# Kernel optimization log

Hardware: AMD Instinct MI355X
Metric: run time of the kernel (lower is better)

Reference implementation:

```python
import jax, jax.numpy as jnp
import numpy as np

E = 1024; H = 16; D = E // H; L = 16
B = 4; TB = 1024; TW = 512
SCALE = D ** -0.5


def _rel_matrix(S):
    r = jnp.arange(S)
    return jnp.clip(r[None, :] - r[:, None], -L, L) + L  # [S,S] ints in [0, 2L]


def _heads(x):
    # [T, b, E] -> [b*H, T, D]
    T, b, _ = x.shape
    return x.reshape(T, b * H, D).transpose(1, 0, 2)


def _rel_logits(q, table, S):
    # Shaw-style relative-key logits without materializing [S,S,D] embeddings:
    # q: [n, S, D], table: [2L+1, D] -> [n, S, S]
    mat = _rel_matrix(S)                          # [S, S]
    all_r = jnp.einsum('ntd,rd->ntr', q, table)   # [n, S, 2L+1]
    return jnp.take_along_axis(all_r, mat[None, :, :], axis=2)


def setup_inputs() -> dict:
    key = jax.random.key(0)
    ks = jax.random.split(key, 10)
    s = 0.02
    w = lambda k, shape: jax.random.normal(k, shape, jnp.float32) * s
    return {
        'query_bpe': jax.random.normal(ks[0], (TB, B, E), jnp.float32),
        'query_word': jax.random.normal(ks[1], (TW, B, E), jnp.float32),
        'mapping': jax.random.uniform(ks[2], (B, TB, TW), jnp.float32),
        'Wq_bpe': w(ks[3], (E, E)), 'bq_bpe': jnp.zeros((E,), jnp.float32),
        'Wk_bpe': w(ks[4], (E, E)), 'bk_bpe': jnp.zeros((E,), jnp.float32),
        'Wq_word': w(ks[5], (E, E)), 'bq_word': jnp.zeros((E,), jnp.float32),
        'Wk_word': w(ks[6], (E, E)), 'bk_word': jnp.zeros((E,), jnp.float32),
        'Wv': w(ks[7], (E, E)), 'bv': jnp.zeros((E,), jnp.float32),
        'Wo': w(ks[8], (E, E)), 'bo': jnp.zeros((E,), jnp.float32),
        'rel_keys_bpe': w(ks[9], (2 * L + 1, D)),
    }


def reference(query_bpe, query_word, mapping, Wq_bpe, bq_bpe, Wk_bpe, bk_bpe,
              Wq_word, bq_word, Wk_word, bk_word, Wv, bv, Wo, bo, rel_keys_bpe):
    b = query_bpe.shape[1]
    q_bpe = _heads((query_bpe @ Wq_bpe.T + bq_bpe) * SCALE)    # [bH, TB, D]
    k_bpe = _heads(query_bpe @ Wk_bpe.T + bk_bpe)
    q_word = _heads((query_word @ Wq_word.T + bq_word) * SCALE)  # [bH, TW, D]
    k_word = _heads(query_word @ Wk_word.T + bk_word)
    v = _heads(query_bpe @ Wv.T + bv)
    # content + relative-position logits for both streams
    # (k_only path in source looks up relative_position_keys_bpe for BOTH streams)
    attn_bpe = q_bpe @ k_bpe.transpose(0, 2, 1) + _rel_logits(q_bpe, rel_keys_bpe, TB)
    attn_word = q_word @ k_word.transpose(0, 2, 1) + _rel_logits(q_word, rel_keys_bpe, TW)
    aw = attn_word.reshape(b, H, TW, TW)
    # fuse word-level scores into BPE positions via alignment mapping: M A M^T
    fused = jnp.einsum('bqw,bhws->bhqs', mapping, aw)
    fused = jnp.einsum('bhqs,bks->bhqk', fused, mapping)
    attn = attn_bpe.reshape(b, H, TB, TB) + fused
    probs = jax.nn.softmax(attn, axis=-1)
    out = jnp.einsum('bhqk,bhkd->bhqd', probs, v.reshape(b, H, TB, D))
    out = out.transpose(2, 0, 1, 3).reshape(TB, b, E)  # back to [T, B, E]
    return out @ Wo.T + bo
```

## Files before the change

kernel.cpp:

```cpp
#include <hip/hip_runtime.h>


#define DEV __device__ __forceinline__
#define GAS(x) ((const __attribute__((address_space(1))) unsigned*)(x))
#define LAS(x) ((__attribute__((address_space(3))) unsigned*)(x))

typedef unsigned short u16;
typedef __attribute__((ext_vector_type(8))) short short8;
typedef __attribute__((ext_vector_type(8))) _Float16 half8;
typedef __attribute__((ext_vector_type(4))) float floatx4;

DEV float bf2f(u16 u) { union { unsigned u; float f; } v; v.u = ((unsigned)u) << 16; return v.f; }
DEV u16 f2bf(float f) {
  union { float f; unsigned u; } v; v.f = f;
  unsigned r = v.u + 0x7FFFu + ((v.u >> 16) & 1u);
  return (u16)(r >> 16);
}
DEV u16 f2h_bits(float f) { union { _Float16 h; u16 u; } v; v.h = (_Float16)f; return v.u; }

template <int N> DEV void vmwait() {
  asm volatile("s_waitcnt vmcnt(%0)" ::"n"(N) : "memory");
  __builtin_amdgcn_sched_barrier(0);
}
DEV void barrier_raw() {
  asm volatile("" ::: "memory");
  __builtin_amdgcn_s_barrier();
  asm volatile("" ::: "memory");
}

DEV void stage_u16(const u16* g, int ld, u16* lds, int tid) {
#pragma unroll
  for (int p = 0; p < 2; ++p) {
    int o = (p * 256 + tid) * 16;
    int r = o >> 6, c = (o >> 4) & 3, sc = c ^ ((r >> 1) & 3);
    __builtin_amdgcn_global_load_lds(GAS(g + (size_t)r * ld + sc * 8),
                                     LAS((char*)lds + o), 16, 0, 0);
  }
}

DEV void stage_u16_half(const u16* g, int ld, u16* lds, int tid, int p) {
  int o = (p * 256 + tid) * 16;
  int r = o >> 6, c = (o >> 4) & 3, sc = c ^ ((r >> 1) & 3);
  __builtin_amdgcn_global_load_lds(GAS(g + (size_t)(r - p * 64) * ld + sc * 8),
                                   LAS((char*)lds + o), 16, 0, 0);
}

DEV void stage_f32_bf(const float* g, int ld, u16* lds, int tid) {
#pragma unroll
  for (int p = 0; p < 2; ++p) {
    int o = (p * 256 + tid) * 16;
    int r = o >> 6, c = (o >> 4) & 3, sc = c ^ ((r >> 1) & 3);
    const float* src = g + (size_t)r * ld + sc * 8;
    union { short8 s; u16 u[8]; } oh;
#pragma unroll
    for (int j = 0; j < 8; ++j) oh.u[j] = f2bf(src[j]);
    *(short8*)((char*)lds + o) = oh.s;
  }
}

DEV void stage_f32_split(const float* g, int ld, u16* ldsh, u16* ldsl, int tid) {
#pragma unroll
  for (int p = 0; p < 2; ++p) {
    int o = (p * 256 + tid) * 16;
    int r = o >> 6, c = (o >> 4) & 3, sc = c ^ ((r >> 1) & 3);
    const float* src = g + (size_t)r * ld + sc * 8;
    union { short8 s; u16 u[8]; } oh, ol;
#pragma unroll
    for (int j = 0; j < 8; ++j) {
      float f = src[j];
      u16 h = f2bf(f);
      oh.u[j] = h;
      ol.u[j] = f2bf(f - bf2f(h));
    }
    *(short8*)((char*)ldsh + o) = oh.s;
    *(short8*)((char*)ldsl + o) = ol.s;
  }
}

DEV short8 frag_ld(const u16* lds, int row, int quad) {
  int c = quad ^ ((row >> 1) & 3);
  return *(const short8*)(lds + row * 32 + c * 8);
}

DEV void mma_bf16(const u16* As, const u16* Bs, int wr, int wc, int m, int quad, floatx4 acc[4][4]) {
  short8 af[4], bf[4];
#pragma unroll
  for (int t = 0; t < 4; ++t) af[t] = frag_ld(As, wr * 64 + t * 16 + m, quad);
#pragma unroll
  for (int t = 0; t < 4; ++t) bf[t] = frag_ld(Bs, wc * 64 + t * 16 + m, quad);
#pragma unroll
  for (int rt = 0; rt < 4; ++rt)
#pragma unroll
    for (int ct = 0; ct < 4; ++ct)
      acc[rt][ct] = __builtin_amdgcn_mfma_f32_16x16x32_bf16(af[rt], bf[ct], acc[rt][ct], 0, 0, 0);
}

DEV void mma_f16(const u16* As, const u16* Bs, int wr, int wc, int m, int quad, floatx4 acc[4][4]) {
  union { short8 s; half8 h; } af[4], bf[4];
#pragma unroll
  for (int t = 0; t < 4; ++t) af[t].s = frag_ld(As, wr * 64 + t * 16 + m, quad);
#pragma unroll
  for (int t = 0; t < 4; ++t) bf[t].s = frag_ld(Bs, wc * 64 + t * 16 + m, quad);
#pragma unroll
  for (int rt = 0; rt < 4; ++rt)
#pragma unroll
    for (int ct = 0; ct < 4; ++ct)
      acc[rt][ct] = __builtin_amdgcn_mfma_f32_16x16x32_f16(af[rt].h, bf[ct].h, acc[rt][ct], 0, 0, 0);
}

DEV void mma_split(const u16* AsH, const u16* AsL, const u16* BsH, const u16* BsL,
                   int wr, int wc, int m, int quad, floatx4 acc[4][4]) {
  short8 ah[4], al[4], bh[4], bl[4];
#pragma unroll
  for (int t = 0; t < 4; ++t) {
    ah[t] = frag_ld(AsH, wr * 64 + t * 16 + m, quad);
    al[t] = frag_ld(AsL, wr * 64 + t * 16 + m, quad);
    bh[t] = frag_ld(BsH, wc * 64 + t * 16 + m, quad);
    bl[t] = frag_ld(BsL, wc * 64 + t * 16 + m, quad);
  }
#pragma unroll
  for (int rt = 0; rt < 4; ++rt)
#pragma unroll
    for (int ct = 0; ct < 4; ++ct) {
      acc[rt][ct] = __builtin_amdgcn_mfma_f32_16x16x32_bf16(ah[rt], bh[ct], acc[rt][ct], 0, 0, 0);
      acc[rt][ct] = __builtin_amdgcn_mfma_f32_16x16x32_bf16(ah[rt], bl[ct], acc[rt][ct], 0, 0, 0);
      acc[rt][ct] = __builtin_amdgcn_mfma_f32_16x16x32_bf16(al[rt], bh[ct], acc[rt][ct], 0, 0, 0);
    }
}

DEV void acc_zero(floatx4 acc[4][4]) {
  floatx4 z = {0.f, 0.f, 0.f, 0.f};
#pragma unroll
  for (int i = 0; i < 4; ++i)
#pragma unroll
    for (int j = 0; j < 4; ++j) acc[i][j] = z;
}

struct CvtB { const float* src[5]; u16* dst[5]; int n8[5]; };
__global__ __launch_bounds__(256) void cvt_bf_kernel(CvtB a) {
  int z = blockIdx.z;
  int i = blockIdx.x * 256 + threadIdx.x;
  if (i >= a.n8[z]) return;
  const float* s = a.src[z] + (size_t)i * 8;
  union { short8 v; u16 u[8]; } o;
#pragma unroll
  for (int j = 0; j < 8; ++j) o.u[j] = f2bf(s[j]);
  *(short8*)(a.dst[z] + (size_t)i * 8) = o.v;
}

struct CvtS { const float* src[3]; u16* dh[3]; u16* dl[3]; int n8[3]; };
__global__ __launch_bounds__(256) void cvt_split_kernel(CvtS a) {
  int z = blockIdx.z;
  int i = blockIdx.x * 256 + threadIdx.x;
  if (i >= a.n8[z]) return;
  const float* s = a.src[z] + (size_t)i * 8;
  union { short8 v; u16 u[8]; } oh, ol;
#pragma unroll
  for (int j = 0; j < 8; ++j) {
    float f = s[j];
    u16 h = f2bf(f);
    oh.u[j] = h;
    ol.u[j] = f2bf(f - bf2f(h));
  }
  *(short8*)(a.dh[z] + (size_t)i * 8) = oh.v;
  *(short8*)(a.dl[z] + (size_t)i * 8) = ol.v;
}

struct PAll {
  const float* Xf[5]; const float* Wf[5];
  const u16* Xh[5]; const u16* Xl[5]; const u16* Wh[5]; const u16* Wl[5];
  const float* bias[5]; float scale[5];
  u16* dh[5]; u16* dl[5]; int T[5]; int md[5]; int prep;
};

__global__ __launch_bounds__(256) void proj_md01_kernel(PAll a) {
  const int z = blockIdx.z;
  __shared__ __align__(16) u16 POOL[16640];
  auto LB = [&](int i) -> u16* { return POOL + i * 4096; };
  const int tid = threadIdx.x;
  const int lane = tid & 63, wv = tid >> 6, wr = wv >> 1, wc = wv & 1;
  const int m = lane & 15, quad = lane >> 4;
  const int md = a.md[z], prep = a.prep;
  const int p = blockIdx.x + 8 * blockIdx.y;
  const int bx = (p >> 3) & 7, by = (p & 7) + 8 * (p >> 6);
  const size_t arow = (size_t)by * 128 * 1024;
  const size_t brow = (size_t)bx * 128 * 1024;
  floatx4 acc[4][4];
  acc_zero(acc);
  if (prep) {
    const u16* Xh = a.Xh[z]; const u16* Wh = a.Wh[z];
    stage_u16(Xh + arow, 1024, LB(0), tid);
    stage_u16(Wh + brow, 1024, LB(1), tid);
    for (int k0 = 0; k0 < 1024; k0 += 32) {
      int o = ((k0 >> 5) & 1) * 2;
      if (k0 + 32 < 1024) {
        int no = 2 - o;
        stage_u16(Xh + arow + k0 + 32, 1024, LB(no), tid);
        stage_u16(Wh + brow + k0 + 32, 1024, LB(no + 1), tid);
        vmwait<4>();
      } else vmwait<0>();
      barrier_raw();
      mma_bf16(LB(o), LB(o + 1), wr, wc, m, quad, acc);
      barrier_raw();
    }
  } else {
    for (int k0 = 0; k0 < 1024; k0 += 32) {
      __syncthreads();
      stage_f32_bf(a.Xf[z] + arow + k0, 1024, LB(0), tid);
      stage_f32_bf(a.Wf[z] + brow + k0, 1024, LB(2), tid);
      __syncthreads();
      mma_bf16(LB(0), LB(2), wr, wc, m, quad, acc);
    }
    __syncthreads();
  }
  const float scale = a.scale[z];
  const float* bias = a.bias[z];
  u16* dh = a.dh[z];
  const int row0l = wr * 64 + quad * 4;
  const int col0l = wc * 64 + m;
  u16* TB = POOL;
  __syncthreads();
#pragma unroll
  for (int rt = 0; rt < 4; ++rt)
#pragma unroll
    for (int ct = 0; ct < 4; ++ct) {
      int cl = col0l + ct * 16;
      float bi = bias[bx * 128 + cl];
#pragma unroll
      for (int rg = 0; rg < 4; ++rg) {
        int rl = row0l + rt * 16 + rg;
        TB[(size_t)cl * 130 + rl] = f2bf((acc[rt][ct][rg] + bi) * scale);
      }
    }
  __syncthreads();
  if (md == 0) {
    int t_local = tid & 31, nloc = tid >> 5;
    int bb = nloc >> 1, hl = nloc & 1;
    int n = bb * 16 + bx * 2 + hl;
    int rl = t_local * 4 + bb;
    size_t base = ((size_t)n * 1024 + by * 32 + t_local) * 64;
#pragma unroll
    for (int g = 0; g < 8; ++g) {
      union { short8 v; u16 u[8]; } o;
#pragma unroll
      for (int j = 0; j < 8; ++j) o.u[j] = TB[(size_t)(hl * 64 + g * 8 + j) * 130 + rl];
      *(short8*)(dh + base + g * 8) = o.v;
    }
  } else {
    for (int task = tid; task < 512; task += 256) {
      int c = task & 127, bb = task >> 7;
      int colg = bx * 128 + c, h = colg >> 6, d = colg & 63;
      size_t base = (((size_t)(bb * 16 + h)) * 64 + d) * 1024 + (size_t)by * 32;
#pragma unroll
      for (int g = 0; g < 4; ++g) {
        union { short8 v; u16 u[8]; } o;
#pragma unroll
        for (int j = 0; j < 8; ++j) o.u[j] = TB[(size_t)c * 130 + bb + 4 * (g * 8 + j)];
        *(short8*)(dh + base + g * 8) = o.v;
      }
    }
  }
}

__global__ __launch_bounds__(256) void proj_md2_kernel(PAll a) {
  const int z = blockIdx.z + 3;
  __shared__ __align__(16) u16 POOL[32768];
  auto LB = [&](int i) -> u16* { return POOL + i * 4096; };
  const int tid = threadIdx.x;
  const int lane = tid & 63, wv = tid >> 6, wr = wv >> 1, wc = wv & 1;
  const int m = lane & 15, quad = lane >> 4;
  const int prep = a.prep;
  const int p = blockIdx.x + 8 * blockIdx.y;
  const int bx = (p >> 3) & 7, by = (p & 7) + 8 * (p >> 6);
  const size_t arow = (size_t)by * 128 * 1024;
  const size_t brow = (size_t)bx * 128 * 1024;
  floatx4 acc[4][4];
  acc_zero(acc);
  if (prep) {
    const u16* Xh = a.Xh[z]; const u16* Xl = a.Xl[z];
    const u16* Wh = a.Wh[z]; const u16* Wl = a.Wl[z];
    stage_u16(Xh + arow, 1024, LB(0), tid);
    stage_u16(Wh + brow, 1024, LB(1), tid);
    stage_u16(Xl + arow, 1024, LB(2), tid);
    stage_u16(Wl + brow, 1024, LB(3), tid);
    for (int k0 = 0; k0 < 1024; k0 += 32) {
      int o = ((k0 >> 5) & 1) * 4;
      if (k0 + 32 < 1024) {
        int no = 4 - o;
        stage_u16(Xh + arow + k0 + 32, 1024, LB(no), tid);
        stage_u16(Wh + brow + k0 + 32, 1024, LB(no + 1), tid);
        stage_u16(Xl + arow + k0 + 32, 1024, LB(no + 2), tid);
        stage_u16(Wl + brow + k0 + 32, 1024, LB(no + 3), tid);
        vmwait<8>();
      } else vmwait<0>();
      barrier_raw();
      mma_split(LB(o), LB(o + 2), LB(o + 1), LB(o + 3), wr, wc, m, quad, acc);
      barrier_raw();
    }
  } else {
    for (int k0 = 0; k0 < 1024; k0 += 32) {
      __syncthreads();
      stage_f32_split(a.Xf[z] + arow + k0, 1024, LB(0), LB(4), tid);
      stage_f32_split(a.Wf[z] + brow + k0, 1024, LB(2), LB(6), tid);
      __syncthreads();
      mma_split(LB(0), LB(4), LB(2), LB(6), wr, wc, m, quad, acc);
    }
    __syncthreads();
  }
  const float scale = a.scale[z];
  const float* bias = a.bias[z];
  u16* dh = a.dh[z];
  u16* dl = a.dl[z];
  const int row0l = wr * 64 + quad * 4;
  u16* TBh = POOL;
  u16* TBl = POOL + 64 * 130;
  for (int pass = 0; pass < 2; ++pass) {
    __syncthreads();
    if (wc == pass) {
#pragma unroll
      for (int rt = 0; rt < 4; ++rt)
#pragma unroll
        for (int ct = 0; ct < 4; ++ct) {
          int cl = ct * 16 + m;
          float bi = bias[bx * 128 + pass * 64 + cl];
#pragma unroll
          for (int rg = 0; rg < 4; ++rg) {
            int rl = row0l + rt * 16 + rg;
            float val = (acc[rt][ct][rg] + bi) * scale;
            u16 hh = f2bf(val);
            TBh[(size_t)cl * 130 + rl] = hh;
            TBl[(size_t)cl * 130 + rl] = f2bf(val - bf2f(hh));
          }
        }
    }
    __syncthreads();
    int c2 = tid & 63, bb = tid >> 6;
    int colg = bx * 128 + pass * 64 + c2, h = colg >> 6, d = colg & 63;
    size_t base = (((size_t)(bb * 16 + h)) * 64 + d) * 512 + (size_t)by * 32;
#pragma unroll
    for (int g = 0; g < 4; ++g) {
      union { short8 v; u16 u[8]; } oh, ol;
#pragma unroll
      for (int j = 0; j < 8; ++j) {
        oh.u[j] = TBh[(size_t)c2 * 130 + bb + 4 * (g * 8 + j)];
        ol.u[j] = TBl[(size_t)c2 * 130 + bb + 4 * (g * 8 + j)];
      }
      *(short8*)(dh + base + g * 8) = oh.v;
      *(short8*)(dl + base + g * 8) = ol.v;
    }
  }
}

__global__ __launch_bounds__(256) void msplit_kernel(const float* __restrict__ M,
                                                     u16* __restrict__ Mh, u16* __restrict__ Ml,
                                                     u16* __restrict__ Mf) {
  int i = blockIdx.x * 256 + threadIdx.x;
  float f = M[i];
  u16 h = f2bf(f);
  Mh[i] = h;
  Ml[i] = f2bf(f - bf2f(h));
  Mf[i] = f2h_bits(f);
}

__global__ __launch_bounds__(256) void rel_bpe_kernel(const u16* __restrict__ q,
                                                      const float* __restrict__ relk,
                                                      float* __restrict__ R) {
  int nt = blockIdx.x * 256 + threadIdx.x;
  float qv[64];
#pragma unroll
  for (int c = 0; c < 8; ++c) {
    union { short8 s; u16 u[8]; } uh; uh.s = *(const short8*)(q + (size_t)nt * 64 + c * 8);
#pragma unroll
    for (int j = 0; j < 8; ++j) qv[c * 8 + j] = bf2f(uh.u[j]);
  }
  for (int r = 0; r < 33; ++r) {
    const float* krow = relk + r * 64;
    float s = 0.f;
#pragma unroll
    for (int d = 0; d < 64; ++d) s += qv[d] * krow[d];
    R[(size_t)nt * 33 + r] = s;
  }
}

__global__ __launch_bounds__(256) void rel_word_kernel(const u16* __restrict__ qh, const u16* __restrict__ ql,
                                                       const float* __restrict__ relk,
                                                       float* __restrict__ R) {
  int nt = blockIdx.x * 256 + threadIdx.x;
  int n = nt >> 9, w = nt & 511;
  float qv[64];
#pragma unroll
  for (int d = 0; d < 64; ++d) {
    size_t idx = ((size_t)n * 64 + d) * 512 + w;
    qv[d] = bf2f(qh[idx]) + bf2f(ql[idx]);
  }
  for (int r = 0; r < 33; ++r) {
    const float* krow = relk + r * 64;
    float s = 0.f;
#pragma unroll
    for (int d = 0; d < 64; ++d) s += qv[d] * krow[d];
    R[(size_t)nt * 33 + r] = s;
  }
}

__global__ __launch_bounds__(256) void relprefix_kernel(const float* __restrict__ Rw,
                                                        const u16* __restrict__ Mf,
                                                        u16* __restrict__ RT,
                                                        float* __restrict__ PS,
                                                        int NCx, int n0) {
  const int bx = blockIdx.x;
  if (bx < NCx * 16) {
    int i = bx * 256 + threadIdx.x;
    int w8 = i & 7, s = (i >> 3) & 31, t = (i >> 8) & 15, nl = i >> 12;
    int n = n0 + nl;
    int w0 = (t == 0) ? 0 : (t == 15 ? 448 : 32 * t - 16);
    int sg = t * 32 + s;
    const float* R = Rw + (size_t)n * 512 * 33;
    union { short8 v; u16 u[8]; } o;
#pragma unroll
    for (int j = 0; j < 8; ++j) {
      int w = w0 + w8 * 8 + j;
      int d = sg - w; d = d < -16 ? -16 : (d > 16 ? 16 : d);
      o.u[j] = f2h_bits(R[(size_t)w * 33 + d + 16]);
    }
    *(short8*)(RT + (size_t)i * 8) = o.v;
  } else {
    const int px = bx - NCx * 16;
    const int nl = px >> 2, n = n0 + nl, b = n >> 4;
    const int q = (px & 3) * 256 + threadIdx.x;
    const u16* mrow = Mf + ((size_t)b * 1024 + q) * 512;
    const float* R = Rw + (size_t)n * 512 * 33;
    float* ps = PS + ((size_t)nl * 1024 + q) * 66;
    float blkA[32], blkB[32];
#pragma unroll
    for (int t = 0; t < 32; ++t) {
      float a = 0.f, bb = 0.f;
#pragma unroll
      for (int c = 0; c < 2; ++c) {
        union { short8 s; _Float16 h[8]; } u;
        u.s = *(const short8*)(mrow + t * 16 + c * 8);
#pragma unroll
        for (int j = 0; j < 8; ++j) {
          int w = t * 16 + c * 8 + j;
          float mv = (float)u.h[j];
          a += mv * R[(size_t)w * 33 + 32];
          bb += mv * R[(size_t)w * 33];
        }
      }
      blkA[t] = a; blkB[t] = bb;
    }
    float run = 0.f;
#pragma unroll
    for (int i = 0; i < 33; ++i) { ps[i] = run; if (i < 32) run += blkA[i]; }
    float tot = 0.f;
#pragma unroll
    for (int i = 0; i < 32; ++i) tot += blkB[i];
    run = tot;
#pragma unroll
    for (int i = 0; i < 33; ++i) { ps[33 + i] = run; if (i < 32) run -= blkB[i]; }
  }
}

__global__ __launch_bounds__(256) void stage1band_kernel(const u16* __restrict__ Mf,
                                                         const u16* __restrict__ RT,
                                                         const float* __restrict__ PS,
                                                         u16* __restrict__ C1r, int n0) {
  __shared__ __align__(16) u16 As0[4096], As1[4096], Bs0[1024], Bs1[1024];
  const int tid = threadIdx.x, qy = blockIdx.x, t = blockIdx.y;
  const int nl = blockIdx.z, n = n0 + nl, b = n >> 4;
  const int lane = tid & 63, wv = tid >> 6;
  const int m = lane & 15, quad = lane >> 4;
  const int w0 = (t == 0) ? 0 : (t == 15 ? 448 : 32 * t - 16);
  const size_t ma = ((size_t)b * 1024 + qy * 128) * 512 + w0;
  const u16* rt = RT + ((size_t)nl * 16 + t) * 2048;
  stage_u16(Mf + ma, 512, As0, tid);
  stage_u16(Mf + ma + 32, 512, As1, tid);
  {
    int half = tid >> 7, tt = tid & 127, o = tt * 16;
    int r = o >> 6, c = (o >> 4) & 3, sc = c ^ ((r >> 1) & 3);
    u16* bs = half ? Bs1 : Bs0;
    __builtin_amdgcn_global_load_lds(GAS(rt + half * 32 + (size_t)r * 64 + sc * 8),
                                     LAS((char*)bs + o), 16, 0, 0);
  }
  floatx4 acc[2][2];
  floatx4 z = {0.f, 0.f, 0.f, 0.f};
  acc[0][0] = z; acc[0][1] = z; acc[1][0] = z; acc[1][1] = z;
  __syncthreads();
#pragma unroll
  for (int ks = 0; ks < 2; ++ks) {
    const u16* As = ks ? As1 : As0;
    const u16* Bs = ks ? Bs1 : Bs0;
    union { short8 s; half8 h; } af[2], bf[2];
#pragma unroll
    for (int i = 0; i < 2; ++i) af[i].s = frag_ld(As, wv * 32 + i * 16 + m, quad);
#pragma unroll
    for (int i = 0; i < 2; ++i) bf[i].s = frag_ld(Bs, i * 16 + m, quad);
#pragma unroll
    for (int i = 0; i < 2; ++i)
#pragma unroll
      for (int j = 0; j < 2; ++j)
        acc[i][j] = __builtin_amdgcn_mfma_f32_16x16x32_f16(af[i].h, bf[j].h, acc[i][j], 0, 0, 0);
  }
  const int ia = w0 >> 4, ib = (w0 + 64) >> 4;
  const float* ps = PS + ((size_t)nl * 1024 + qy * 128) * 66;
#pragma unroll
  for (int i = 0; i < 2; ++i)
#pragma unroll
    for (int rg = 0; rg < 4; ++rg) {
      int row = wv * 32 + i * 16 + quad * 4 + rg;
      float ab = ps[(size_t)row * 66 + ia] + ps[(size_t)row * 66 + 33 + ib];
      int q = qy * 128 + row;
#pragma unroll
      for (int j = 0; j < 2; ++j) {
        int s = t * 32 + j * 16 + m;
        C1r[((size_t)nl * 1024 + q) * 512 + s] = f2h_bits(acc[i][j][rg] + ab);
      }
    }
}

__global__ __launch_bounds__(256) void mqk_kernel(const u16* __restrict__ Mh, const u16* __restrict__ Ml,
                                                  const u16* __restrict__ qwTh, const u16* __restrict__ qwTl,
                                                  const u16* __restrict__ kwTh, const u16* __restrict__ kwTl,
                                                  u16* __restrict__ MQh, u16* __restrict__ MQl,
                                                  u16* __restrict__ MKh, u16* __restrict__ MKl, int n0) {
  __shared__ __align__(16) u16 POOL[32768];
  auto LB = [&](int i) -> u16* { return POOL + i * 4096; };
  const int tid = threadIdx.x, nl = blockIdx.y, n = n0 + nl, b = n >> 4;
  const int lane = tid & 63, wv = tid >> 6, wr = wv >> 1, wc = wv & 1;
  const int m = lane & 15, quad = lane >> 4;
  const size_t ma = ((size_t)b * 1024 + blockIdx.x * 128) * 512;
  const u16* Qh = qwTh + (size_t)n * 32768;
  const u16* Ql = qwTl + (size_t)n * 32768;
  const u16* Kh = kwTh + (size_t)n * 32768;
  const u16* Kl = kwTl + (size_t)n * 32768;
  floatx4 acc[4][4];
  acc_zero(acc);
  auto stage_set = [&](int o, int k) {
    stage_u16(Mh + ma + k, 512, LB(o), tid);
    stage_u16(Ml + ma + k, 512, LB(o + 1), tid);
    stage_u16_half(Qh + k, 512, LB(o + 2), tid, 0);
    stage_u16_half(Kh + k, 512, LB(o + 2), tid, 1);
    stage_u16_half(Ql + k, 512, LB(o + 3), tid, 0);
    stage_u16_half(Kl + k, 512, LB(o + 3), tid, 1);
  };
  stage_set(0, 0);
  for (int k0 = 0; k0 < 512; k0 += 32) {
    int o = ((k0 >> 5) & 1) * 4;
    if (k0 + 32 < 512) {
      stage_set(4 - o, k0 + 32);
      vmwait<8>();
    } else vmwait<0>();
    barrier_raw();
    mma_split(LB(o), LB(o + 1), LB(o + 2), LB(o + 3), wr, wc, m, quad, acc);
    barrier_raw();
  }
  u16* dsth = wc ? MKh : MQh;
  u16* dstl = wc ? MKl : MQl;
  const int row0 = blockIdx.x * 128 + wr * 64 + quad * 4;
#pragma unroll
  for (int rt = 0; rt < 4; ++rt)
#pragma unroll
    for (int ct = 0; ct < 4; ++ct) {
      int d = (ct * 16 + m) & 63;
#pragma unroll
      for (int rg = 0; rg < 4; ++rg) {
        int row = row0 + rt * 16 + rg;
        size_t idx = ((size_t)nl * 1024 + row) * 64 + d;
        float val = acc[rt][ct][rg];
        u16 hh = f2bf(val);
        dsth[idx] = hh;
        dstl[idx] = f2bf(val - bf2f(hh));
      }
    }
}

__global__ __launch_bounds__(256) void logits_kernel(const u16* __restrict__ qb, const u16* __restrict__ kb,
                                                     const u16* __restrict__ MQh, const u16* __restrict__ MQl,
                                                     const u16* __restrict__ MKh, const u16* __restrict__ MKl,
                                                     const u16* __restrict__ C1r, const u16* __restrict__ Mf,
                                                     const float* __restrict__ Rb, u16* __restrict__ L,
                                                     int n0) {
  __shared__ __align__(16) u16 POOL[16384];
  auto LB = [&](int i) -> u16* { return POOL + i * 4096; };
  const int tid = threadIdx.x, nl = blockIdx.z, n = n0 + nl, b = n >> 4;
  const int bq = blockIdx.x, bk = blockIdx.y;
  const int lane = tid & 63, wv = tid >> 6, wr = wv >> 1, wc = wv & 1;
  const int m = lane & 15, quad = lane >> 4;
  const size_t qa = ((size_t)n * 1024 + bq * 128) * 64;
  const size_t ka = ((size_t)n * 1024 + bk * 128) * 64;
  const size_t mqa = ((size_t)nl * 1024 + bq * 128) * 64;
  const size_t mka = ((size_t)nl * 1024 + bk * 128) * 64;
  const size_t ca = ((size_t)nl * 1024 + bq * 128) * 512;
  const size_t ma = ((size_t)b * 1024 + bk * 128) * 512;
  floatx4 acc[4][4];
  acc_zero(acc);
  stage_u16(qb + qa, 64, LB(0), tid);
  stage_u16(kb + ka, 64, LB(1), tid);
  __syncthreads();
  stage_u16(qb + qa + 32, 64, LB(2), tid);
  stage_u16(kb + ka + 32, 64, LB(3), tid);
  mma_bf16(LB(0), LB(1), wr, wc, m, quad, acc);
  __syncthreads();
  mma_bf16(LB(2), LB(3), wr, wc, m, quad, acc);
  __syncthreads();
#pragma unroll
  for (int k0 = 0; k0 < 64; k0 += 32) {
    stage_u16(MQh + mqa + k0, 64, LB(0), tid);
    stage_u16(MQl + mqa + k0, 64, LB(1), tid);
    stage_u16(MKh + mka + k0, 64, LB(2), tid);
    stage_u16(MKl + mka + k0, 64, LB(3), tid);
    __syncthreads();
    mma_split(LB(0), LB(1), LB(2), LB(3), wr, wc, m, quad, acc);
    __syncthreads();
  }
  stage_u16(C1r + ca, 512, LB(0), tid);
  stage_u16(Mf + ma, 512, LB(1), tid);
  for (int k0 = 0; k0 < 512; k0 += 32) {
    int o = ((k0 >> 5) & 1) * 2;
    if (k0 + 32 < 512) {
      int no = 2 - o;
      stage_u16(C1r + ca + k0 + 32, 512, LB(no), tid);
      stage_u16(Mf + ma + k0 + 32, 512, LB(no + 1), tid);
      vmwait<4>();
    } else vmwait<0>();
    barrier_raw();
    mma_f16(LB(o), LB(o + 1), wr, wc, m, quad, acc);
    barrier_raw();
  }
  const int q0 = bq * 128 + wr * 64 + quad * 4;
  const int k0c = bk * 128 + wc * 64 + m;
#pragma unroll
  for (int rt = 0; rt < 4; ++rt)
#pragma unroll
    for (int ct = 0; ct < 4; ++ct) {
      int kc = k0c + ct * 16;
#pragma unroll
      for (int rg = 0; rg < 4; ++rg) {
        int q = q0 + rt * 16 + rg;
        int id = kc - q; id = id < -16 ? -16 : (id > 16 ? 16 : id); id += 16;
        float val = acc[rt][ct][rg] + Rb[((size_t)n * 1024 + q) * 33 + id];
        L[((size_t)nl * 1024 + q) * 1024 + kc] = f2h_bits(val);
      }
    }
}

__global__ __launch_bounds__(256) void softmax_pv_kernel(const u16* __restrict__ L,
                                                         const u16* __restrict__ VT,
                                                         u16* __restrict__ AO, int NCk, int n0) {
  __shared__ __align__(16) u16 Vs[2][4][2048];
  const int tid = threadIdx.x, lane = tid & 63, wv = tid >> 6;
  const int m = lane & 15, quad = lane >> 4;
  int qt, nl;
  if (NCk >= 8) {
    int lin = blockIdx.x + 16 * blockIdx.y;
    int xcd = lin & 7, j = lin >> 3;
    qt = j & 15;
    nl = xcd + 8 * (j >> 4);
  } else { qt = blockIdx.x; nl = blockIdx.y; }
  const int n = n0 + nl;
  const int qrow = qt * 64 + wv * 16 + m;
  const u16* Lrow = L + ((size_t)nl * 1024 + qrow) * 1024;
  const u16* Vbase = VT + (size_t)n * 64 * 1024;
  float mi = -1e30f, li = 0.f;
  floatx4 O[4];
  floatx4 z = {0.f, 0.f, 0.f, 0.f};
#pragma unroll
  for (int dt = 0; dt < 4; ++dt) O[dt] = z;

  auto stageV = [&](int kt, int buf) {
#pragma unroll
    for (int ct = 0; ct < 4; ++ct) {
      int o = tid * 16;
      int r = o >> 6, c = (o >> 4) & 3, sc = c ^ ((r >> 1) & 3);
      __builtin_amdgcn_global_load_lds(GAS(Vbase + (size_t)r * 1024 + kt * 128 + ct * 32 + sc * 8),
                                       LAS((char*)Vs[buf][ct] + o), 16, 0, 0);
    }
  };
  stageV(0, 0);

  for (int kt = 0; kt < 8; ++kt) {
    int cur = kt & 1;

    float vals[4][8];
#pragma unroll
    for (int ct = 0; ct < 4; ++ct) {
      union { short8 s; _Float16 h[8]; } u;
      u.s = *(const short8*)(Lrow + kt * 128 + ct * 32 + quad * 8);
#pragma unroll
      for (int j = 0; j < 8; ++j) vals[ct][j] = (float)u.h[j];
    }
    float tmax = vals[0][0];
#pragma unroll
    for (int ct = 0; ct < 4; ++ct)
#pragma unroll
      for (int j = 0; j < 8; ++j) tmax = fmaxf(tmax, vals[ct][j]);
    tmax = fmaxf(tmax, __shfl_xor(tmax, 16));
    tmax = fmaxf(tmax, __shfl_xor(tmax, 32));
    float mnew = fmaxf(mi, tmax);
    float alpha = __expf(mi - mnew);
    float pv[4][8];
    float tsum = 0.f;
#pragma unroll
    for (int ct = 0; ct < 4; ++ct)
#pragma unroll
      for (int j = 0; j < 8; ++j) { pv[ct][j] = __expf(vals[ct][j] - mnew); tsum += pv[ct][j]; }
    tsum += __shfl_xor(tsum, 16);
    tsum += __shfl_xor(tsum, 32);
    li = li * alpha + tsum;
    mi = mnew;

    if (kt + 1 < 8) { stageV(kt + 1, cur ^ 1); vmwait<4>(); }
    else vmwait<0>();
    barrier_raw();

    float ar[4];
#pragma unroll
    for (int rg = 0; rg < 4; ++rg) ar[rg] = __shfl(alpha, quad * 4 + rg);
#pragma unroll
    for (int dt = 0; dt < 4; ++dt)
#pragma unroll
      for (int rg = 0; rg < 4; ++rg) O[dt][rg] *= ar[rg];

    short8 pf[4];
#pragma unroll
    for (int ct = 0; ct < 4; ++ct) {
      union { short8 s; u16 us[8]; } up;
#pragma unroll
      for (int j = 0; j < 8; ++j) up.us[j] = f2bf(pv[ct][j]);
      pf[ct] = up.s;
    }
#pragma unroll
    for (int ct = 0; ct < 4; ++ct)
#pragma unroll
      for (int dt = 0; dt < 4; ++dt) {
        short8 vf = frag_ld(Vs[cur][ct], dt * 16 + m, quad);
        O[dt] = __builtin_amdgcn_mfma_f32_16x16x32_bf16(pf[ct], vf, O[dt], 0, 0, 0);
      }
    barrier_raw();
  }

  float linv = 1.f / li;
  float lr[4];
#pragma unroll
  for (int rg = 0; rg < 4; ++rg) lr[rg] = __shfl(linv, quad * 4 + rg);
  const int b = n >> 4, h = n & 15;
#pragma unroll
  for (int dt = 0; dt < 4; ++dt)
#pragma unroll
    for (int rg = 0; rg < 4; ++rg) {
      int q = qt * 64 + wv * 16 + quad * 4 + rg;
      float ov = O[dt][rg] * lr[rg];
      AO[((size_t)q * 4 + b) * 1024 + h * 64 + dt * 16 + m] = f2bf(ov);
    }
}

__global__ __launch_bounds__(256) void outproj_kernel(const u16* __restrict__ AO, const float* __restrict__ Wo,
                                                      const u16* __restrict__ Wob, int prep,
                                                      const float* __restrict__ bo, float* __restrict__ out) {
  __shared__ __align__(16) u16 POOL[16384];
  auto LB = [&](int i) -> u16* { return POOL + i * 4096; };
  const int tid = threadIdx.x;
  const int lane = tid & 63, wv = tid >> 6, wr = wv >> 1, wc = wv & 1;
  const int m = lane & 15, quad = lane >> 4;
  const int p = blockIdx.x + 8 * blockIdx.y;
  const int bx = (p >> 3) & 7, by = (p & 7) + 8 * (p >> 6);
  const u16* A = AO + (size_t)by * 128 * 1024;
  const size_t brow = (size_t)bx * 128 * 1024;
  floatx4 acc[4][4];
  acc_zero(acc);
  if (prep) {
    stage_u16(A, 1024, LB(0), tid);
    stage_u16(Wob + brow, 1024, LB(1), tid);
    for (int k0 = 0; k0 < 1024; k0 += 32) {
      int o = ((k0 >> 5) & 1) * 2;
      if (k0 + 32 < 1024) {
        int no = 2 - o;
        stage_u16(A + k0 + 32, 1024, LB(no), tid);
        stage_u16(Wob + brow + k0 + 32, 1024, LB(no + 1), tid);
        vmwait<4>();
      } else vmwait<0>();
      barrier_raw();
      mma_bf16(LB(o), LB(o + 1), wr, wc, m, quad, acc);
      barrier_raw();
    }
  } else {
    for (int k0 = 0; k0 < 1024; k0 += 32) {
      __syncthreads();
      stage_u16(A + k0, 1024, LB(0), tid);
      stage_f32_bf(Wo + brow + k0, 1024, LB(2), tid);
      __syncthreads();
      mma_bf16(LB(0), LB(2), wr, wc, m, quad, acc);
    }
  }
  const int r0 = by * 128 + wr * 64 + quad * 4;
  const int c0 = bx * 128 + wc * 64 + m;
#pragma unroll
  for (int rt = 0; rt < 4; ++rt)
#pragma unroll
    for (int ct = 0; ct < 4; ++ct) {
      int col = c0 + ct * 16;
      float bi = bo[col];
#pragma unroll
      for (int rg = 0; rg < 4; ++rg) {
        int row = r0 + rt * 16 + rg;
        out[(size_t)row * 1024 + col] = acc[rt][ct][rg] + bi;
      }
    }
}

extern "C" void kernel_launch(void* const* d_in, const int* in_sizes, int n_in,
                              void* d_out, int out_size, void* d_ws, size_t ws_size,
                              hipStream_t stream) {
  const float* query_bpe = (const float*)d_in[0];
  const float* query_word = (const float*)d_in[1];
  const float* mapping = (const float*)d_in[2];
  const float* Wq_bpe = (const float*)d_in[3];
  const float* bq_bpe = (const float*)d_in[4];
  const float* Wk_bpe = (const float*)d_in[5];
  const float* bk_bpe = (const float*)d_in[6];
  const float* Wq_word = (const float*)d_in[7];
  const float* bq_word = (const float*)d_in[8];
  const float* Wk_word = (const float*)d_in[9];
  const float* bk_word = (const float*)d_in[10];
  const float* Wv = (const float*)d_in[11];
  const float* bv = (const float*)d_in[12];
  const float* Wo = (const float*)d_in[13];
  const float* bo = (const float*)d_in[14];
  const float* relk = (const float*)d_in[15];

  char* ws = (char*)d_ws;
  size_t off = 0;
  u16* q_bpe = (u16*)(ws + off); off += 8388608;
  u16* k_bpe = (u16*)(ws + off); off += 8388608;
  u16* VTb   = (u16*)(ws + off); off += 8388608;
  u16* qwT_h = (u16*)(ws + off); off += 4194304;
  u16* qwT_l = (u16*)(ws + off); off += 4194304;
  u16* kwT_h = (u16*)(ws + off); off += 4194304;
  u16* kwT_l = (u16*)(ws + off); off += 4194304;
  u16* M_h   = (u16*)(ws + off); off += 4194304;
  u16* M_l   = (u16*)(ws + off); off += 4194304;
  u16* M_f   = (u16*)(ws + off); off += 4194304;
  float* R_word = (float*)(ws + off); off += 4325376;
  float* R_bpe  = (float*)(ws + off); off += 8650752;
  u16* AO    = (u16*)(ws + off); off += 8388608;
  u16* Wo_bf = (u16*)(ws + off); off += 2097152;
  const size_t fixed_end = off;

  const size_t avail = (ws_size > fixed_end) ? ws_size - fixed_end : 0;
  const int prep = avail >= 31457280 ? 1 : 0;
  const size_t per_nc = 4005888;
  int NC = 1;
  for (int c = 64; c >= 1; c >>= 1) {
    if ((size_t)c * per_nc <= avail) { NC = c; break; }
  }
  char* vb = ws + fixed_end;
  u16* RelT  = (u16*)(vb);
  float* PS  = (float*)(vb + (size_t)NC * 65536);
  u16* C1r   = (u16*)(vb + (size_t)NC * 335872);
  u16* L_c   = (u16*)(vb + (size_t)NC * 1384448);
  u16* MQh   = (u16*)(vb + (size_t)NC * 3481600);
  u16* MQl   = (u16*)(vb + (size_t)NC * 3612672);
  u16* MKh   = (u16*)(vb + (size_t)NC * 3743744);
  u16* MKl   = (u16*)(vb + (size_t)NC * 3874816);
  u16* Xb    = (u16*)(vb);
  u16* Wqb   = (u16*)(vb + 8388608);
  u16* Wkb   = (u16*)(vb + 10485760);
  u16* Wvb   = (u16*)(vb + 12582912);
  u16* Xw_h  = (u16*)(vb + 14680064);
  u16* Xw_l  = (u16*)(vb + 18874368);
  u16* Wqw_h = (u16*)(vb + 23068672);
  u16* Wqw_l = (u16*)(vb + 25165824);
  u16* Wkw_h = (u16*)(vb + 27262976);
  u16* Wkw_l = (u16*)(vb + 29360128);

  if (prep) {
    CvtB cb = {};
    cb.src[0] = query_bpe; cb.dst[0] = Xb;    cb.n8[0] = 524288;
    cb.src[1] = Wq_bpe;    cb.dst[1] = Wqb;   cb.n8[1] = 131072;
    cb.src[2] = Wk_bpe;    cb.dst[2] = Wkb;   cb.n8[2] = 131072;
    cb.src[3] = Wv;        cb.dst[3] = Wvb;   cb.n8[3] = 131072;
    cb.src[4] = Wo;        cb.dst[4] = Wo_bf; cb.n8[4] = 131072;
    cvt_bf_kernel<<<dim3(2048, 1, 5), 256, 0, stream>>>(cb);
    CvtS cs = {};
    cs.src[0] = query_word; cs.dh[0] = Xw_h;  cs.dl[0] = Xw_l;  cs.n8[0] = 262144;
    cs.src[1] = Wq_word;    cs.dh[1] = Wqw_h; cs.dl[1] = Wqw_l; cs.n8[1] = 131072;
    cs.src[2] = Wk_word;    cs.dh[2] = Wkw_h; cs.dl[2] = Wkw_l; cs.n8[2] = 131072;
    cvt_split_kernel<<<dim3(1024, 1, 3), 256, 0, stream>>>(cs);
  }

  PAll pa = {};
  pa.prep = prep;
  pa.Xf[0] = query_bpe;  pa.Wf[0] = Wq_bpe;  pa.Xh[0] = Xb;   pa.Wh[0] = Wqb;
  pa.bias[0] = bq_bpe;  pa.scale[0] = 0.125f; pa.dh[0] = q_bpe; pa.T[0] = 1024; pa.md[0] = 0;
  pa.Xf[1] = query_bpe;  pa.Wf[1] = Wk_bpe;  pa.Xh[1] = Xb;   pa.Wh[1] = Wkb;
  pa.bias[1] = bk_bpe;  pa.scale[1] = 1.0f;   pa.dh[1] = k_bpe; pa.T[1] = 1024; pa.md[1] = 0;
  pa.Xf[2] = query_bpe;  pa.Wf[2] = Wv;      pa.Xh[2] = Xb;   pa.Wh[2] = Wvb;
  pa.bias[2] = bv;      pa.scale[2] = 1.0f;   pa.dh[2] = VTb;   pa.T[2] = 1024; pa.md[2] = 1;
  pa.Xf[3] = query_word; pa.Wf[3] = Wq_word; pa.Xh[3] = Xw_h; pa.Xl[3] = Xw_l;
  pa.Wh[3] = Wqw_h; pa.Wl[3] = Wqw_l;
  pa.bias[3] = bq_word; pa.scale[3] = 0.125f; pa.dh[3] = qwT_h; pa.dl[3] = qwT_l; pa.T[3] = 512; pa.md[3] = 2;
  pa.Xf[4] = query_word; pa.Wf[4] = Wk_word; pa.Xh[4] = Xw_h; pa.Xl[4] = Xw_l;
  pa.Wh[4] = Wkw_h; pa.Wl[4] = Wkw_l;
  pa.bias[4] = bk_word; pa.scale[4] = 1.0f;   pa.dh[4] = kwT_h; pa.dl[4] = kwT_l; pa.T[4] = 512; pa.md[4] = 2;
  proj_md01_kernel<<<dim3(8, 32, 3), 256, 0, stream>>>(pa);
  proj_md2_kernel<<<dim3(8, 16, 2), 256, 0, stream>>>(pa);

  msplit_kernel<<<dim3(4 * 1024 * 512 / 256), 256, 0, stream>>>(mapping, M_h, M_l, M_f);

  rel_bpe_kernel<<<dim3(64 * 1024 / 256), 256, 0, stream>>>(q_bpe, relk, R_bpe);
  rel_word_kernel<<<dim3(64 * 512 / 256), 256, 0, stream>>>(qwT_h, qwT_l, relk, R_word);

  for (int n0 = 0; n0 < 64; n0 += NC) {
    relprefix_kernel<<<dim3(NC * 20), 256, 0, stream>>>(R_word, M_f, RelT, PS, NC, n0);
    mqk_kernel<<<dim3(8, NC), 256, 0, stream>>>(M_h, M_l, qwT_h, qwT_l, kwT_h, kwT_l,
                                                MQh, MQl, MKh, MKl, n0);
    stage1band_kernel<<<dim3(8, 16, NC), 256, 0, stream>>>(M_f, RelT, PS, C1r, n0);
    logits_kernel<<<dim3(8, 8, NC), 256, 0, stream>>>(q_bpe, k_bpe, MQh, MQl, MKh, MKl,
                                                      C1r, M_f, R_bpe, L_c, n0);
    softmax_pv_kernel<<<dim3(16, NC), 256, 0, stream>>>(L_c, VTb, AO, NC, n0);
  }

  outproj_kernel<<<dim3(8, 32), 256, 0, stream>>>(AO, Wo, Wo_bf, prep, bo, (float*)d_out);
}
```

Baseline: 596.8 us.

## Fuse logits computation with softmax-PV into flash-style attention kernel

Merges the logits kernel and the softmax/PV kernel into one kernel. Each block owns a 64-row query tile and loops over the 8 key tiles, computing logits into LDS and applying online softmax and the PV product in place. This removes the fp16 global logits buffer write and its re-read, and shrinks per-chunk workspace, which can allow larger NC. The cost is less parallelism (NC×16 blocks instead of NC×64), key tiles recomputed serially per block, and lost V double-buffering overlap.

```diff
diff --git a/kernel.cpp b/kernel.cpp
--- a/kernel.cpp
+++ b/kernel.cpp
@@ -22,6 +22,10 @@
   asm volatile("s_waitcnt vmcnt(%0)" ::"n"(N) : "memory");
   __builtin_amdgcn_sched_barrier(0);
 }
+DEV void lgkmwait0() {
+  asm volatile("s_waitcnt lgkmcnt(0)" ::: "memory");
+  __builtin_amdgcn_sched_barrier(0);
+}
 DEV void barrier_raw() {
   asm volatile("" ::: "memory");
   __builtin_amdgcn_s_barrier();
@@ -38,6 +42,13 @@
   }
 }
 
+DEV void stage_u16_64(const u16* g, int ld, u16* lds, int tid) {
+  int o = tid * 16;
+  int r = o >> 6, c = (o >> 4) & 3, sc = c ^ ((r >> 1) & 3);
+  __builtin_amdgcn_global_load_lds(GAS(g + (size_t)r * ld + sc * 8),
+                                   LAS((char*)lds + o), 16, 0, 0);
+}
+
 DEV void stage_u16_half(const u16* g, int ld, u16* lds, int tid, int p) {
   int o = (p * 256 + tid) * 16;
   int r = o >> 6, c = (o >> 4) & 3, sc = c ^ ((r >> 1) & 3);
@@ -95,19 +106,6 @@
       acc[rt][ct] = __builtin_amdgcn_mfma_f32_16x16x32_bf16(af[rt], bf[ct], acc[rt][ct], 0, 0, 0);
 }
 
-DEV void mma_f16(const u16* As, const u16* Bs, int wr, int wc, int m, int quad, floatx4 acc[4][4]) {
-  union { short8 s; half8 h; } af[4], bf[4];
-#pragma unroll
-  for (int t = 0; t < 4; ++t) af[t].s = frag_ld(As, wr * 64 + t * 16 + m, quad);
-#pragma unroll
-  for (int t = 0; t < 4; ++t) bf[t].s = frag_ld(Bs, wc * 64 + t * 16 + m, quad);
-#pragma unroll
-  for (int rt = 0; rt < 4; ++rt)
-#pragma unroll
-    for (int ct = 0; ct < 4; ++ct)
-      acc[rt][ct] = __builtin_amdgcn_mfma_f32_16x16x32_f16(af[rt].h, bf[ct].h, acc[rt][ct], 0, 0, 0);
-}
-
 DEV void mma_split(const u16* AsH, const u16* AsL, const u16* BsH, const u16* BsL,
                    int wr, int wc, int m, int quad, floatx4 acc[4][4]) {
   short8 ah[4], al[4], bh[4], bl[4];
@@ -120,6 +118,55 @@
   }
 #pragma unroll
   for (int rt = 0; rt < 4; ++rt)
+#pragma unroll
+    for (int ct = 0; ct < 4; ++ct) {
+      acc[rt][ct] = __builtin_amdgcn_mfma_f32_16x16x32_bf16(ah[rt], bh[ct], acc[rt][ct], 0, 0, 0);
+      acc[rt][ct] = __builtin_amdgcn_mfma_f32_16x16x32_bf16(ah[rt], bl[ct], acc[rt][ct], 0, 0, 0);
+      acc[rt][ct] = __builtin_amdgcn_mfma_f32_16x16x32_bf16(al[rt], bh[ct], acc[rt][ct], 0, 0, 0);
+    }
+}
+
+DEV void mma64_bf16(const u16* As, const u16* Bs, int wr, int wc, int m, int quad, floatx4 acc[2][4]) {
+  short8 af[2], bf[4];
+#pragma unroll
+  for (int t = 0; t < 2; ++t) af[t] = frag_ld(As, wr * 32 + t * 16 + m, quad);
+#pragma unroll
+  for (int t = 0; t < 4; ++t) bf[t] = frag_ld(Bs, wc * 64 + t * 16 + m, quad);
+#pragma unroll
+  for (int rt = 0; rt < 2; ++rt)
+#pragma unroll
+    for (int ct = 0; ct < 4; ++ct)
+      acc[rt][ct] = __builtin_amdgcn_mfma_f32_16x16x32_bf16(af[rt], bf[ct], acc[rt][ct], 0, 0, 0);
+}
+
+DEV void mma64_f16(const u16* As, const u16* Bs, int wr, int wc, int m, int quad, floatx4 acc[2][4]) {
+  union { short8 s; half8 h; } af[2], bf[4];
+#pragma unroll
+  for (int t = 0; t < 2; ++t) af[t].s = frag_ld(As, wr * 32 + t * 16 + m, quad);
+#pragma unroll
+  for (int t = 0; t < 4; ++t) bf[t].s = frag_ld(Bs, wc * 64 + t * 16 + m, quad);
+#pragma unroll
+  for (int rt = 0; rt < 2; ++rt)
+#pragma unroll
+    for (int ct = 0; ct < 4; ++ct)
+      acc[rt][ct] = __builtin_amdgcn_mfma_f32_16x16x32_f16(af[rt].h, bf[ct].h, acc[rt][ct], 0, 0, 0);
+}
+
+DEV void mma64_split(const u16* AsH, const u16* AsL, const u16* BsH, const u16* BsL,
+                     int wr, int wc, int m, int quad, floatx4 acc[2][4]) {
+  short8 ah[2], al[2], bh[4], bl[4];
+#pragma unroll
+  for (int t = 0; t < 2; ++t) {
+    ah[t] = frag_ld(AsH, wr * 32 + t * 16 + m, quad);
+    al[t] = frag_ld(AsL, wr * 32 + t * 16 + m, quad);
+  }
+#pragma unroll
+  for (int t = 0; t < 4; ++t) {
+    bh[t] = frag_ld(BsH, wc * 64 + t * 16 + m, quad);
+    bl[t] = frag_ld(BsL, wc * 64 + t * 16 + m, quad);
+  }
+#pragma unroll
+  for (int rt = 0; rt < 2; ++rt)
 #pragma unroll
     for (int ct = 0; ct < 4; ++ct) {
       acc[rt][ct] = __builtin_amdgcn_mfma_f32_16x16x32_bf16(ah[rt], bh[ct], acc[rt][ct], 0, 0, 0);
@@ -573,118 +620,107 @@
     }
 }
 
-__global__ __launch_bounds__(256) void logits_kernel(const u16* __restrict__ qb, const u16* __restrict__ kb,
-                                                     const u16* __restrict__ MQh, const u16* __restrict__ MQl,
-                                                     const u16* __restrict__ MKh, const u16* __restrict__ MKl,
-                                                     const u16* __restrict__ C1r, const u16* __restrict__ Mf,
-                                                     const float* __restrict__ Rb, u16* __restrict__ L,
-                                                     int n0) {
-  __shared__ __align__(16) u16 POOL[16384];
-  auto LB = [&](int i) -> u16* { return POOL + i * 4096; };
-  const int tid = threadIdx.x, nl = blockIdx.z, n = n0 + nl, b = n >> 4;
-  const int bq = blockIdx.x, bk = blockIdx.y;
+__global__ __launch_bounds__(256) void fused_attn_kernel(
+    const u16* __restrict__ qb, const u16* __restrict__ kb,
+    const u16* __restrict__ MQh, const u16* __restrict__ MQl,
+    const u16* __restrict__ MKh, const u16* __restrict__ MKl,
+    const u16* __restrict__ C1r, const u16* __restrict__ Mf,
+    const float* __restrict__ Rb, const u16* __restrict__ VT,
+    u16* __restrict__ AO, int n0) {
+  __shared__ __align__(16) u16 POOL[12288];
+  __shared__ __align__(16) u16 Vs[4][2048];
+  u16* A0 = POOL; u16* A1 = POOL + 2048; u16* B0 = POOL + 4096; u16* B1 = POOL + 8192;
+  u16* Ltile = POOL;
+  const int tid = threadIdx.x;
   const int lane = tid & 63, wv = tid >> 6, wr = wv >> 1, wc = wv & 1;
   const int m = lane & 15, quad = lane >> 4;
-  const size_t qa = ((size_t)n * 1024 + bq * 128) * 64;
-  const size_t ka = ((size_t)n * 1024 + bk * 128) * 64;
-  const size_t mqa = ((size_t)nl * 1024 + bq * 128) * 64;
-  const size_t mka = ((size_t)nl * 1024 + bk * 128) * 64;
-  const size_t ca = ((size_t)nl * 1024 + bq * 128) * 512;
-  const size_t ma = ((size_t)b * 1024 + bk * 128) * 512;
-  floatx4 acc[4][4];
-  acc_zero(acc);
-  stage_u16(qb + qa, 64, LB(0), tid);
-  stage_u16(kb + ka, 64, LB(1), tid);
-  __syncthreads();
-  stage_u16(qb + qa + 32, 64, LB(2), tid);
-  stage_u16(kb + ka + 32, 64, LB(3), tid);
-  mma_bf16(LB(0), LB(1), wr, wc, m, quad, acc);
-  __syncthreads();
-  mma_bf16(LB(2), LB(3), wr, wc, m, quad, acc);
-  __syncthreads();
-#pragma unroll
-  for (int k0 = 0; k0 < 64; k0 += 32) {
-    stage_u16(MQh + mqa + k0, 64, LB(0), tid);
-    stage_u16(MQl + mqa + k0, 64, LB(1), tid);
-    stage_u16(MKh + mka + k0, 64, LB(2), tid);
-    stage_u16(MKl + mka + k0, 64, LB(3), tid);
-    __syncthreads();
-    mma_split(LB(0), LB(1), LB(2), LB(3), wr, wc, m, quad, acc);
-    __syncthreads();
-  }
-  stage_u16(C1r + ca, 512, LB(0), tid);
-  stage_u16(Mf + ma, 512, LB(1), tid);
-  for (int k0 = 0; k0 < 512; k0 += 32) {
-    int o = ((k0 >> 5) & 1) * 2;
-    if (k0 + 32 < 512) {
-      int no = 2 - o;
-      stage_u16(C1r + ca + k0 + 32, 512, LB(no), tid);
-      stage_u16(Mf + ma + k0 + 32, 512, LB(no + 1), tid);
-      vmwait<4>();
-    } else vmwait<0>();
-    barrier_raw();
-    mma_f16(LB(o), LB(o + 1), wr, wc, m, quad, acc);
-    barrier_raw();
-  }
-  const int q0 = bq * 128 + wr * 64 + quad * 4;
-  const int k0c = bk * 128 + wc * 64 + m;
-#pragma unroll
-  for (int rt = 0; rt < 4; ++rt)
-#pragma unroll
-    for (int ct = 0; ct < 4; ++ct) {
-      int kc = k0c + ct * 16;
-#pragma unroll
-      for (int rg = 0; rg < 4; ++rg) {
-        int q = q0 + rt * 16 + rg;
-        int id = kc - q; id = id < -16 ? -16 : (id > 16 ? 16 : id); id += 16;
-        float val = acc[rt][ct][rg] + Rb[((size_t)n * 1024 + q) * 33 + id];
-        L[((size_t)nl * 1024 + q) * 1024 + kc] = f2h_bits(val);
-      }
-    }
-}
-
-__global__ __launch_bounds__(256) void softmax_pv_kernel(const u16* __restrict__ L,
-                                                         const u16* __restrict__ VT,
-                                                         u16* __restrict__ AO, int NCk, int n0) {
-  __shared__ __align__(16) u16 Vs[2][4][2048];
-  const int tid = threadIdx.x, lane = tid & 63, wv = tid >> 6;
-  const int m = lane & 15, quad = lane >> 4;
-  int qt, nl;
-  if (NCk >= 8) {
-    int lin = blockIdx.x + 16 * blockIdx.y;
-    int xcd = lin & 7, j = lin >> 3;
-    qt = j & 15;
-    nl = xcd + 8 * (j >> 4);
-  } else { qt = blockIdx.x; nl = blockIdx.y; }
-  const int n = n0 + nl;
-  const int qrow = qt * 64 + wv * 16 + m;
-  const u16* Lrow = L + ((size_t)nl * 1024 + qrow) * 1024;
+  const int nl = blockIdx.x, bq = blockIdx.y, n = n0 + nl, b = n >> 4;
+  const size_t qa  = ((size_t)n * 1024 + bq * 64) * 64;
+  const size_t mqa = ((size_t)nl * 1024 + bq * 64) * 64;
+  const size_t ca  = ((size_t)nl * 1024 + bq * 64) * 512;
   const u16* Vbase = VT + (size_t)n * 64 * 1024;
+
   float mi = -1e30f, li = 0.f;
   floatx4 O[4];
-  floatx4 z = {0.f, 0.f, 0.f, 0.f};
-#pragma unroll
-  for (int dt = 0; dt < 4; ++dt) O[dt] = z;
-
-  auto stageV = [&](int kt, int buf) {
+  {
+    floatx4 z = {0.f, 0.f, 0.f, 0.f};
+#pragma unroll
+    for (int dt = 0; dt < 4; ++dt) O[dt] = z;
+  }
+
+  for (int bk = 0; bk < 8; ++bk) {
+    const size_t ka  = ((size_t)n * 1024 + bk * 128) * 64;
+    const size_t mka = ((size_t)nl * 1024 + bk * 128) * 64;
+    const size_t ma  = ((size_t)b * 1024 + bk * 128) * 512;
+    floatx4 acc[2][4];
+    {
+      floatx4 z = {0.f, 0.f, 0.f, 0.f};
+#pragma unroll
+      for (int rt = 0; rt < 2; ++rt)
+#pragma unroll
+        for (int ct = 0; ct < 4; ++ct) acc[rt][ct] = z;
+    }
+    stage_u16_64(qb + qa, 64, A0, tid);
+    stage_u16_64(qb + qa + 32, 64, A1, tid);
+    stage_u16(kb + ka, 64, B0, tid);
+    stage_u16(kb + ka + 32, 64, B1, tid);
+    __syncthreads();
+    mma64_bf16(A0, B0, wr, wc, m, quad, acc);
+    mma64_bf16(A1, B1, wr, wc, m, quad, acc);
+    __syncthreads();
+#pragma unroll
+    for (int k0 = 0; k0 < 64; k0 += 32) {
+      stage_u16_64(MQh + mqa + k0, 64, A0, tid);
+      stage_u16_64(MQl + mqa + k0, 64, A1, tid);
+      stage_u16(MKh + mka + k0, 64, B0, tid);
+      stage_u16(MKl + mka + k0, 64, B1, tid);
+      __syncthreads();
+      mma64_split(A0, A1, B0, B1, wr, wc, m, quad, acc);
+      __syncthreads();
+    }
+    stage_u16_64(C1r + ca, 512, A0, tid);
+    stage_u16(Mf + ma, 512, B0, tid);
+    for (int k0 = 0; k0 < 512; k0 += 32) {
+      int odd = (k0 >> 5) & 1;
+      if (k0 + 32 < 512) {
+        stage_u16_64(C1r + ca + k0 + 32, 512, odd ? A0 : A1, tid);
+        stage_u16(Mf + ma + k0 + 32, 512, odd ? B0 : B1, tid);
+        vmwait<3>();
+      } else vmwait<0>();
+      barrier_raw();
+      mma64_f16(odd ? A1 : A0, odd ? B1 : B0, wr, wc, m, quad, acc);
+      barrier_raw();
+    }
+#pragma unroll
+    for (int rt = 0; rt < 2; ++rt)
+#pragma unroll
+      for (int ct = 0; ct < 4; ++ct) {
+        int col = wc * 64 + ct * 16 + m;
+        int kc = bk * 128 + col;
+#pragma unroll
+        for (int rg = 0; rg < 4; ++rg) {
+          int row = wr * 32 + rt * 16 + quad * 4 + rg;
+          int q = bq * 64 + row;
+          int id = kc - q; id = id < -16 ? -16 : (id > 16 ? 16 : id); id += 16;
+          float val = acc[rt][ct][rg] + Rb[((size_t)n * 1024 + q) * 33 + id];
+          Ltile[(size_t)row * 136 + col] = f2h_bits(val);
+        }
+      }
 #pragma unroll
     for (int ct = 0; ct < 4; ++ct) {
       int o = tid * 16;
       int r = o >> 6, c = (o >> 4) & 3, sc = c ^ ((r >> 1) & 3);
-      __builtin_amdgcn_global_load_lds(GAS(Vbase + (size_t)r * 1024 + kt * 128 + ct * 32 + sc * 8),
-                                       LAS((char*)Vs[buf][ct] + o), 16, 0, 0);
-    }
-  };
-  stageV(0, 0);
-
-  for (int kt = 0; kt < 8; ++kt) {
-    int cur = kt & 1;
-
+      __builtin_amdgcn_global_load_lds(GAS(Vbase + (size_t)r * 1024 + bk * 128 + ct * 32 + sc * 8),
+                                       LAS((char*)Vs[ct] + o), 16, 0, 0);
+    }
+    lgkmwait0();
+    barrier_raw();
+    const int row = wv * 16 + m;
     float vals[4][8];
 #pragma unroll
     for (int ct = 0; ct < 4; ++ct) {
       union { short8 s; _Float16 h[8]; } u;
-      u.s = *(const short8*)(Lrow + kt * 128 + ct * 32 + quad * 8);
+      u.s = *(const short8*)(Ltile + (size_t)row * 136 + ct * 32 + quad * 8);
 #pragma unroll
       for (int j = 0; j < 8; ++j) vals[ct][j] = (float)u.h[j];
     }
@@ -707,19 +743,13 @@
     tsum += __shfl_xor(tsum, 32);
     li = li * alpha + tsum;
     mi = mnew;
-
-    if (kt + 1 < 8) { stageV(kt + 1, cur ^ 1); vmwait<4>(); }
-    else vmwait<0>();
-    barrier_raw();
-
-    float ar[4];
-#pragma unroll
-    for (int rg = 0; rg < 4; ++rg) ar[rg] = __shfl(alpha, quad * 4 + rg);
+    float alr[4];
+#pragma unroll
+    for (int rg = 0; rg < 4; ++rg) alr[rg] = __shfl(alpha, quad * 4 + rg);
 #pragma unroll
     for (int dt = 0; dt < 4; ++dt)
 #pragma unroll
-      for (int rg = 0; rg < 4; ++rg) O[dt][rg] *= ar[rg];
-
+      for (int rg = 0; rg < 4; ++rg) O[dt][rg] *= alr[rg];
     short8 pf[4];
 #pragma unroll
     for (int ct = 0; ct < 4; ++ct) {
@@ -728,28 +758,30 @@
       for (int j = 0; j < 8; ++j) up.us[j] = f2bf(pv[ct][j]);
       pf[ct] = up.s;
     }
+    vmwait<0>();
+    barrier_raw();
 #pragma unroll
     for (int ct = 0; ct < 4; ++ct)
 #pragma unroll
       for (int dt = 0; dt < 4; ++dt) {
-        short8 vf = frag_ld(Vs[cur][ct], dt * 16 + m, quad);
+        short8 vf = frag_ld(Vs[ct], dt * 16 + m, quad);
         O[dt] = __builtin_amdgcn_mfma_f32_16x16x32_bf16(pf[ct], vf, O[dt], 0, 0, 0);
       }
     barrier_raw();
   }
 
+  const int hb = n & 15;
   float linv = 1.f / li;
   float lr[4];
 #pragma unroll
   for (int rg = 0; rg < 4; ++rg) lr[rg] = __shfl(linv, quad * 4 + rg);
-  const int b = n >> 4, h = n & 15;
 #pragma unroll
   for (int dt = 0; dt < 4; ++dt)
 #pragma unroll
     for (int rg = 0; rg < 4; ++rg) {
-      int q = qt * 64 + wv * 16 + quad * 4 + rg;
+      int q = bq * 64 + wv * 16 + quad * 4 + rg;
       float ov = O[dt][rg] * lr[rg];
-      AO[((size_t)q * 4 + b) * 1024 + h * 64 + dt * 16 + m] = f2bf(ov);
+      AO[((size_t)q * 4 + b) * 1024 + hb * 64 + dt * 16 + m] = f2bf(ov);
     }
 }
 
@@ -847,7 +879,7 @@
 
   const size_t avail = (ws_size > fixed_end) ? ws_size - fixed_end : 0;
   const int prep = avail >= 31457280 ? 1 : 0;
-  const size_t per_nc = 4005888;
+  const size_t per_nc = 1908736;
   int NC = 1;
   for (int c = 64; c >= 1; c >>= 1) {
     if ((size_t)c * per_nc <= avail) { NC = c; break; }
@@ -856,11 +888,10 @@
   u16* RelT  = (u16*)(vb);
   float* PS  = (float*)(vb + (size_t)NC * 65536);
   u16* C1r   = (u16*)(vb + (size_t)NC * 335872);
-  u16* L_c   = (u16*)(vb + (size_t)NC * 1384448);
-  u16* MQh   = (u16*)(vb + (size_t)NC * 3481600);
-  u16* MQl   = (u16*)(vb + (size_t)NC * 3612672);
-  u16* MKh   = (u16*)(vb + (size_t)NC * 3743744);
-  u16* MKl   = (u16*)(vb + (size_t)NC * 3874816);
+  u16* MQh   = (u16*)(vb + (size_t)NC * 1384448);
+  u16* MQl   = (u16*)(vb + (size_t)NC * 1515520);
+  u16* MKh   = (u16*)(vb + (size_t)NC * 1646592);
+  u16* MKl   = (u16*)(vb + (size_t)NC * 1777664);
   u16* Xb    = (u16*)(vb);
   u16* Wqb   = (u16*)(vb + 8388608);
   u16* Wkb   = (u16*)(vb + 10485760);
@@ -914,9 +945,8 @@
     mqk_kernel<<<dim3(8, NC), 256, 0, stream>>>(M_h, M_l, qwT_h, qwT_l, kwT_h, kwT_l,
                                                 MQh, MQl, MKh, MKl, n0);
     stage1band_kernel<<<dim3(8, 16, NC), 256, 0, stream>>>(M_f, RelT, PS, C1r, n0);
-    logits_kernel<<<dim3(8, 8, NC), 256, 0, stream>>>(q_bpe, k_bpe, MQh, MQl, MKh, MKl,
-                                                      C1r, M_f, R_bpe, L_c, n0);
-    softmax_pv_kernel<<<dim3(16, NC), 256, 0, stream>>>(L_c, VTb, AO, NC, n0);
+    fused_attn_kernel<<<dim3(NC, 16), 256, 0, stream>>>(q_bpe, k_bpe, MQh, MQl, MKh, MKl,
+                                                        C1r, M_f, R_bpe, VTb, AO, n0);
   }
 
   outproj_kernel<<<dim3(8, 32), 256, 0, stream>>>(AO, Wo, Wo_bf, prep, bo, (float*)d_out);
```

Result: no change. 601.5 us (+0.8%).
